# Kernel tuning notes

Hardware: AMD Instinct MI355X
Metric: run time of the kernel (lower is better)

The kernel has to match this reference:

```python
import jax, jax.numpy as jnp
import numpy as np

MAXT = 10000
BATCH = 4096
LOG_GAMMA = float(np.log(1.02))
ALPHA = float(np.log(0.99) / 1000.0)
INIT_LOGW = float(np.log(0.248))
INIT_LOGP = float(np.log(0.001))
TEMPERATURE = 1000.0
EPS = 1e-12


def setup_inputs() -> dict:
    key = jax.random.key(0)
    k1, k2 = jax.random.split(key)
    # actions are initialized to -10 in the original module (must be << 0 so exp(a) < 1)
    acts = -10.0 * jnp.ones((MAXT,), dtype=jnp.float32)
    u1 = jax.random.uniform(k1, (MAXT, BATCH), dtype=jnp.float32)
    u2 = jax.random.uniform(k2, (MAXT, BATCH), dtype=jnp.float32)
    return {"acts": acts, "u1": u1, "u2": u2}


def _gumbel_sigmoid(logp, uu1, uu2):
    # logit = logp - log(1 - exp(logp))
    logit = logp - jnp.log1p(-jnp.exp(logp))
    noise = -jnp.log(jnp.log(uu2 + EPS) / jnp.log(uu1 + EPS) + EPS)
    soft = jax.nn.sigmoid(logit + noise)  # gumbel_temp = 1
    hard = (soft > 0.5).astype(soft.dtype)
    # straight-through: hard value, soft gradient
    return soft + jax.lax.stop_gradient(hard - soft)


def reference(acts, u1, u2):
    def step(carry, xs):
        logp, logw, alive, cumrew = carry
        a, uu1, uu2 = xs
        alive = alive * (1.0 - _gumbel_sigmoid(logp, uu1, uu2))
        f = jnp.exp(a)
        new_logw = logw + LOG_GAMMA + jnp.log(1.0 - f)
        new_logp = logp + ALPHA * f * jnp.exp(logw)
        rwd = alive * jnp.exp(new_logw / TEMPERATURE)
        return (new_logp, new_logw, alive, cumrew + rwd), None

    batch = u1.shape[1]
    init = (
        jnp.full((batch,), INIT_LOGP, dtype=jnp.float32),
        jnp.full((batch,), INIT_LOGW, dtype=jnp.float32),
        jnp.ones((batch,), dtype=jnp.float32),
        jnp.zeros((batch,), dtype=jnp.float32),
    )
    (_, _, _, cumrew), _ = jax.lax.scan(step, init, (acts, u1, u2))
    return cumrew.mean()
```

## Files before the change

### kernel.cpp

```cpp
#include <hip/hip_runtime.h>
#include <limits.h>

#define MAXT 10000
#define BATCH 4096
#define NYB 80
#define TCHUNK 16
#define SEGT 1536
#define EPT 6
#define NT2 1024
#define SEG2 10
#define CUT_ODDS 9.3e-13f

#define LOG_GAMMA_C  1.9802627296e-2f
#define ALPHA_C     -1.0050335854e-5f
#define INIT_LOGW_C -1.3943265329f
#define INIT_LOGP_C -6.9077552790f
#define EPS_C        1e-12f

__device__ __forceinline__ float block_exscan_tot(float v, float* sh, int tid,
                                                  int n, float* tot) {
    sh[tid] = v;
    __syncthreads();
    for (int off = 1; off < n; off <<= 1) {
        float x = (tid >= off) ? sh[tid - off] : 0.0f;
        __syncthreads();
        sh[tid] += x;
        __syncthreads();
    }
    float excl = (tid > 0) ? sh[tid - 1] : 0.0f;
    float t_ = sh[n - 1];
    __syncthreads();
    *tot = t_;
    return excl;
}

__global__ __launch_bounds__(256) void scan_fused(
    const float* __restrict__ acts,
    const float* __restrict__ u1, const float* __restrict__ u2,
    unsigned* __restrict__ fftab)
{
    __shared__ float sh[256];
    __shared__ int   shi[256];
    __shared__ float s_gate[SEGT];

    const int tid = threadIdx.x;
    const int b4  = (blockIdx.x * 256 + tid) * 4;
    const float E = EPS_C;

    float carry_w = INIT_LOGW_C;
    float carry_p = INIT_LOGP_C;
    unsigned f0 = MAXT, f1 = MAXT, f2 = MAXT, f3 = MAXT;

    for (int seg_base = 0; seg_base < MAXT; seg_base += SEGT) {
        float fv[EPT], dv[EPT];
        float lsum = 0.0f;
        #pragma unroll
        for (int i = 0; i < EPT; ++i) {
            int t = seg_base + tid * EPT + i;
            if (t < MAXT) {
                float f = expf(acts[t]);
                fv[i] = f;
                dv[i] = LOG_GAMMA_C + logf(1.0f - f);
            } else { fv[i] = 0.0f; dv[i] = 0.0f; }
            lsum += dv[i];
        }
        float dtot;
        float excl = block_exscan_tot(lsum, sh, tid, 256, &dtot);

        float run = carry_w + excl;
        float cv[EPT];
        float csum = 0.0f;
        #pragma unroll
        for (int i = 0; i < EPT; ++i) {
            cv[i] = ALPHA_C * fv[i] * expf(run);
            run += dv[i];
            csum += cv[i];
        }
        float ctot;
        float cexcl = block_exscan_tot(csum, sh, tid, 256, &ctot);

        float logp = carry_p + cexcl;
        int localFirst = INT_MAX;
        #pragma unroll
        for (int i = 0; i < EPT; ++i) {
            int t = seg_base + tid * EPT + i;
            float el   = expf(logp);
            float odds = el / (1.0f - el);
            s_gate[tid * EPT + i] = odds - E;
            if (localFirst == INT_MAX && odds <= CUT_ODDS) localFirst = t;
            logp += cv[i];
        }
        shi[tid] = localFirst;
        __syncthreads();
        for (int off = 128; off > 0; off >>= 1) {
            if (tid < off) shi[tid] = min(shi[tid], shi[tid + off]);
            __syncthreads();
        }
        const int segcut = shi[0];
        __syncthreads();

        const int tlimit = min(segcut, MAXT);
        for (int lc = 0; lc < SEGT / TCHUNK; ++lc) {
            const int cg = seg_base / TCHUNK + lc;
            if ((cg % NYB) != (int)blockIdx.y) continue;
            const int tstart = seg_base + lc * TCHUNK;
            if (tstart >= tlimit) break;
            #pragma unroll
            for (int g = 0; g < TCHUNK / 4; ++g) {
                float4 a[4], c[4];
                float gv[4];
                #pragma unroll
                for (int j = 0; j < 4; ++j) {
                    const int t = tstart + g * 4 + j;
                    a[j]  = *(const float4*)(u1 + (size_t)t * BATCH + b4);
                    c[j]  = *(const float4*)(u2 + (size_t)t * BATCH + b4);
                    gv[j] = s_gate[t - seg_base];
                }
                #pragma unroll
                for (int j = 0; j < 4; ++j) {
                    const unsigned t = (unsigned)(tstart + g * 4 + j);
                    const float k = gv[j];
                    if (__logf(c[j].x + E) > k * __logf(a[j].x + E)) f0 = min(f0, t);
                    if (__logf(c[j].y + E) > k * __logf(a[j].y + E)) f1 = min(f1, t);
                    if (__logf(c[j].z + E) > k * __logf(a[j].z + E)) f2 = min(f2, t);
                    if (__logf(c[j].w + E) > k * __logf(a[j].w + E)) f3 = min(f3, t);
                }
            }
        }

        if (segcut != INT_MAX) break;
        carry_w += dtot;
        carry_p += ctot;
        __syncthreads();
    }

    uint4 outv; outv.x = f0; outv.y = f1; outv.z = f2; outv.w = f3;
    *(uint4*)(fftab + (size_t)blockIdx.y * BATCH + b4) = outv;
}

__global__ __launch_bounds__(NT2) void finalize_kernel(
    const float* __restrict__ acts,
    const unsigned* __restrict__ fftab,
    float* __restrict__ out)
{
    __shared__ float  sh[NT2];
    __shared__ float  rp[MAXT + 1];
    __shared__ double sd[NT2];
    const int tid = threadIdx.x;

    const int t0 = tid * SEG2;
    const int n  = (t0 < MAXT) ? min(SEG2, MAXT - t0) : 0;

    float dv[SEG2];
    float lsum = 0.0f;
    for (int i = 0; i < n; ++i) {
        float f = expf(acts[t0 + i]);
        dv[i] = LOG_GAMMA_C + logf(1.0f - f);
        lsum += dv[i];
    }
    float dtot;
    float excl = block_exscan_tot(lsum, sh, tid, NT2, &dtot);
    float run = INIT_LOGW_C + excl;

    float rv[SEG2];
    float rsum = 0.0f;
    for (int i = 0; i < n; ++i) {
        run += dv[i];
        rv[i] = expf(run * 1e-3f);
        rsum += rv[i];
    }
    float rtot;
    float rexcl = block_exscan_tot(rsum, sh, tid, NT2, &rtot);
    float rrun = rexcl;
    for (int i = 0; i < n; ++i) { rp[t0 + i] = rrun; rrun += rv[i]; }
    if (tid == 0) rp[MAXT] = rtot;
    __syncthreads();

    double s = 0.0;
    for (int b = tid; b < BATCH; b += NT2) {
        unsigned ff = 0xFFFFFFFFu;
        #pragma unroll 8
        for (int y = 0; y < NYB; ++y) ff = min(ff, fftab[(size_t)y * BATCH + b]);
        int t = (int)min(ff, (unsigned)MAXT);
        s += (double)rp[t];
    }
    sd[tid] = s;
    __syncthreads();
    for (int off = NT2 / 2; off > 0; off >>= 1) {
        if (tid < off) sd[tid] += sd[tid + off];
        __syncthreads();
    }
    if (tid == 0) out[0] = (float)(sd[0] / (double)BATCH);
}

extern "C" void kernel_launch(void* const* d_in, const int* in_sizes, int n_in,
                              void* d_out, int out_size, void* d_ws, size_t ws_size,
                              hipStream_t stream) {
    const float* acts = (const float*)d_in[0];
    const float* u1   = (const float*)d_in[1];
    const float* u2   = (const float*)d_in[2];
    float* out = (float*)d_out;

    unsigned* fftab = (unsigned*)d_ws;

    dim3 grid(BATCH / (256 * 4), NYB);
    scan_fused<<<grid, 256, 0, stream>>>(acts, u1, u2, fftab);
    finalize_kernel<<<1, NT2, 0, stream>>>(acts, fftab, out);
}
```

Before: 293.2 us.

## Replace per-block first-death table with atomicMin and use wave-shuffle reductions

Instead of writing an NYB x BATCH table of first-death times for the finalize kernel to min-reduce, each block does atomicMin into a single BATCH-sized array, initialized by a memset. The shared-memory tree reductions and Hillis-Steele scans are replaced by wave-level shuffle scans and reductions, which need fewer barriers. Together these shrink the serial work in the single-block finalize kernel. In exchange the change adds a memset launch and atomic traffic.

```diff
diff --git a/kernel.cpp b/kernel.cpp
--- a/kernel.cpp
+++ b/kernel.cpp
@@ -34,13 +34,37 @@
     return excl;
 }
 
+__device__ __forceinline__ float block_exscan_tot_fast(float v, float* shw,
+                                                       int tid, int nwaves,
+                                                       float* tot) {
+    float s = v;
+    #pragma unroll
+    for (int o = 1; o < 64; o <<= 1) {
+        float x = __shfl_up(s, o, 64);
+        if ((tid & 63) >= o) s += x;
+    }
+    float sprev = __shfl_up(s, 1, 64);
+    const int wid = tid >> 6, lane = tid & 63;
+    if (lane == 63) shw[wid] = s;
+    __syncthreads();
+    float wpre = 0.0f, wtot = 0.0f;
+    for (int w = 0; w < nwaves; ++w) {
+        float x = shw[w];
+        wtot += x;
+        if (w < wid) wpre += x;
+    }
+    __syncthreads();
+    *tot = wtot;
+    return (lane == 0) ? wpre : (wpre + sprev);
+}
+
 __global__ __launch_bounds__(256) void scan_fused(
     const float* __restrict__ acts,
     const float* __restrict__ u1, const float* __restrict__ u2,
-    unsigned* __restrict__ fftab)
+    unsigned* __restrict__ ff)
 {
     __shared__ float sh[256];
-    __shared__ int   shi[256];
+    __shared__ int   swmin[4];
     __shared__ float s_gate[SEGT];
 
     const int tid = threadIdx.x;
@@ -90,14 +114,13 @@
             if (localFirst == INT_MAX && odds <= CUT_ODDS) localFirst = t;
             logp += cv[i];
         }
-        shi[tid] = localFirst;
-        __syncthreads();
-        for (int off = 128; off > 0; off >>= 1) {
-            if (tid < off) shi[tid] = min(shi[tid], shi[tid + off]);
-            __syncthreads();
-        }
-        const int segcut = shi[0];
-        __syncthreads();
+        #pragma unroll
+        for (int o = 32; o > 0; o >>= 1)
+            localFirst = min(localFirst, __shfl_xor(localFirst, o, 64));
+        if ((tid & 63) == 0) swmin[tid >> 6] = localFirst;
+        __syncthreads();
+        const int segcut = min(min(swmin[0], swmin[1]),
+                               min(swmin[2], swmin[3]));
 
         const int tlimit = min(segcut, MAXT);
         for (int lc = 0; lc < SEGT / TCHUNK; ++lc) {
@@ -134,19 +157,26 @@
         __syncthreads();
     }
 
-    uint4 outv; outv.x = f0; outv.y = f1; outv.z = f2; outv.w = f3;
-    *(uint4*)(fftab + (size_t)blockIdx.y * BATCH + b4) = outv;
+    if (f0 < MAXT) atomicMin(&ff[b4 + 0], f0);
+    if (f1 < MAXT) atomicMin(&ff[b4 + 1], f1);
+    if (f2 < MAXT) atomicMin(&ff[b4 + 2], f2);
+    if (f3 < MAXT) atomicMin(&ff[b4 + 3], f3);
 }
 
 __global__ __launch_bounds__(NT2) void finalize_kernel(
     const float* __restrict__ acts,
-    const unsigned* __restrict__ fftab,
+    const unsigned* __restrict__ ff,
     float* __restrict__ out)
 {
-    __shared__ float  sh[NT2];
+    __shared__ float  shw[16];
+    __shared__ double sdw[16];
     __shared__ float  rp[MAXT + 1];
-    __shared__ double sd[NT2];
     const int tid = threadIdx.x;
+
+    const unsigned fv0 = ff[tid];
+    const unsigned fv1 = ff[tid + NT2];
+    const unsigned fv2 = ff[tid + 2 * NT2];
+    const unsigned fv3 = ff[tid + 3 * NT2];
 
     const int t0 = tid * SEG2;
     const int n  = (t0 < MAXT) ? min(SEG2, MAXT - t0) : 0;
@@ -159,7 +189,7 @@
         lsum += dv[i];
     }
     float dtot;
-    float excl = block_exscan_tot(lsum, sh, tid, NT2, &dtot);
+    float excl = block_exscan_tot_fast(lsum, shw, tid, NT2 / 64, &dtot);
     float run = INIT_LOGW_C + excl;
 
     float rv[SEG2];
@@ -170,27 +200,27 @@
         rsum += rv[i];
     }
     float rtot;
-    float rexcl = block_exscan_tot(rsum, sh, tid, NT2, &rtot);
+    float rexcl = block_exscan_tot_fast(rsum, shw, tid, NT2 / 64, &rtot);
     float rrun = rexcl;
     for (int i = 0; i < n; ++i) { rp[t0 + i] = rrun; rrun += rv[i]; }
     if (tid == 0) rp[MAXT] = rtot;
     __syncthreads();
 
     double s = 0.0;
-    for (int b = tid; b < BATCH; b += NT2) {
-        unsigned ff = 0xFFFFFFFFu;
-        #pragma unroll 8
-        for (int y = 0; y < NYB; ++y) ff = min(ff, fftab[(size_t)y * BATCH + b]);
-        int t = (int)min(ff, (unsigned)MAXT);
-        s += (double)rp[t];
-    }
-    sd[tid] = s;
-    __syncthreads();
-    for (int off = NT2 / 2; off > 0; off >>= 1) {
-        if (tid < off) sd[tid] += sd[tid + off];
-        __syncthreads();
-    }
-    if (tid == 0) out[0] = (float)(sd[0] / (double)BATCH);
+    s += (double)rp[min(fv0, (unsigned)MAXT)];
+    s += (double)rp[min(fv1, (unsigned)MAXT)];
+    s += (double)rp[min(fv2, (unsigned)MAXT)];
+    s += (double)rp[min(fv3, (unsigned)MAXT)];
+
+    #pragma unroll
+    for (int o = 32; o > 0; o >>= 1) s += __shfl_xor(s, o, 64);
+    if ((tid & 63) == 0) sdw[tid >> 6] = s;
+    __syncthreads();
+    if (tid == 0) {
+        double t_ = 0.0;
+        for (int w = 0; w < NT2 / 64; ++w) t_ += sdw[w];
+        out[0] = (float)(t_ / (double)BATCH);
+    }
 }
 
 extern "C" void kernel_launch(void* const* d_in, const int* in_sizes, int n_in,
@@ -201,9 +231,11 @@
     const float* u2   = (const float*)d_in[2];
     float* out = (float*)d_out;
 
-    unsigned* fftab = (unsigned*)d_ws;
+    unsigned* ff = (unsigned*)d_ws;
+
+    hipMemsetAsync(ff, 0xFF, BATCH * sizeof(unsigned), stream);
 
     dim3 grid(BATCH / (256 * 4), NYB);
-    scan_fused<<<grid, 256, 0, stream>>>(acts, u1, u2, fftab);
-    finalize_kernel<<<1, NT2, 0, stream>>>(acts, fftab, out);
-}
+    scan_fused<<<grid, 256, 0, stream>>>(acts, u1, u2, ff);
+    finalize_kernel<<<1, NT2, 0, stream>>>(acts, ff, out);
+}
```

New measurement: 280.5 us. 4.3% less time.
